# Optimization experiments

Hardware: AMD Instinct MI355X
Metric: run time of the kernel (lower is better)

Reference implementation:

```python
import jax, jax.numpy as jnp
import numpy as np


def setup_inputs() -> dict:
    key = jax.random.key(0)
    k1, k2 = jax.random.split(key)
    x = jax.random.normal(k1, (32, 512, 384), dtype=jnp.float32)
    duration = jax.random.randint(k2, (32, 512), 0, 16, dtype=jnp.int32)
    return {"x": x, "duration": duration, "max_len": 4096}


def reference(x, duration, max_len):
    # x: [B, T, D] phoneme encodings; duration: [B, T] nonneg frame counts.
    # Equivalent to repeat_interleave(x, duration, axis=1) then pad/truncate to max_len.
    dur = jnp.maximum(duration, 0)
    cs = jnp.cumsum(dur, axis=1)                      # [B, T] cumulative end offsets
    t = jnp.arange(max_len, dtype=cs.dtype)          # [L] output frame positions
    # frame t belongs to phoneme i iff cs[i-1] <= t < cs[i]
    idx = jax.vmap(lambda c: jnp.searchsorted(c, t, side="right"))(cs)  # [B, L]
    total = cs[:, -1]                                 # [B] expanded lengths (mel_len)
    valid = t[None, :] < total[:, None]               # [B, L] frames beyond total are padding
    idx = jnp.minimum(idx, x.shape[1] - 1)
    out = jnp.take_along_axis(x, idx[:, :, None], axis=1)   # [B, L, D] gather
    out = jnp.where(valid[:, :, None], out, jnp.zeros((), dtype=x.dtype))
    return out, total
```

## Files before the change

### kernel.cpp

```cpp
#include <hip/hip_runtime.h>
#include <hip/hip_bf16.h>


#define B      32
#define S      512
#define T      4096
#define D      384
#define D4     96
#define TILE_T 64

__global__ __launch_bounds__(256) void lr_fused_kernel(
    const float4* __restrict__ x,
    const int*    __restrict__ duration,
    float4*       __restrict__ out,
    float*        __restrict__ total_out)
{
    const int blk = blockIdx.x;
    const int b   = blk >> 6;
    const int t0  = (blk & 63) * TILE_T;
    const int tid = threadIdx.x;

    __shared__ int s_cs[S];
    __shared__ int s_p[256];
    __shared__ int s_idx[TILE_T];

    const int2 d2 = ((const int2*)(duration + b * S))[tid];
    const int a0 = max(d2.x, 0);
    const int a1 = max(d2.y, 0);
    s_p[tid] = a0 + a1;
    __syncthreads();

    #pragma unroll
    for (int off = 1; off < 256; off <<= 1) {
        int v = (tid >= off) ? s_p[tid - off] : 0;
        __syncthreads();
        s_p[tid] += v;
        __syncthreads();
    }

    const int P = s_p[tid];
    s_cs[2 * tid]     = P - a1;
    s_cs[2 * tid + 1] = P;
    __syncthreads();

    const int total = s_cs[S - 1];

    if (t0 == 0 && tid == 0) {
        total_out[b] = (float)total;
    }

    if (tid < TILE_T) {
        const int t = t0 + tid;
        int idx = -1;
        if (t < total) {
            int lo = 0;
            #pragma unroll
            for (int step = 256; step > 0; step >>= 1) {
                int mid = lo + step;
                if (mid <= S && s_cs[mid - 1] <= t) lo = mid;
            }
            idx = min(lo, S - 1);
        }
        s_idx[tid] = idx;
    }
    __syncthreads();

    const float4* xb = x   + (size_t)b * S * D4;
    float4*       ob = out + ((size_t)b * T + t0) * D4;

    #pragma unroll 4
    for (int e = tid; e < TILE_T * D4; e += 256) {
        const int r = e / D4;
        const int c = e - r * D4;
        const int idx = s_idx[r];
        float4 v;
        if (idx < 0) {
            v = make_float4(0.f, 0.f, 0.f, 0.f);
        } else {
            v = xb[idx * D4 + c];
        }
        ob[r * D4 + c] = v;
    }
}

extern "C" void kernel_launch(void* const* d_in, const int* in_sizes, int n_in,
                              void* d_out, int out_size, void* d_ws, size_t ws_size,
                              hipStream_t stream) {
    const float* x        = (const float*)d_in[0];
    const int*   duration = (const int*)d_in[1];

    float* out      = (float*)d_out;
    float* total_of = out + (size_t)B * T * D;

    const int nblocks = B * (T / TILE_T);
    lr_fused_kernel<<<nblocks, 256, 0, stream>>>(
        (const float4*)x, duration, (float4*)out, total_of);
}
```

Before: 40.69 us.

## Use wave-shuffle scan, XCD-aware block remap, larger tiles and nontemporal stores

Replaces the shared-memory Hillis-Steele prefix scan, which needs many barriers, with a wavefront shuffle scan plus a small cross-wave combine. Doubles the time tile to 128 frames so each block does more output work per scan. Remaps block IDs so consecutive logical tiles of a batch land on the same XCD, aiming to improve L2 reuse of the x rows. Writes output with nontemporal stores to avoid polluting cache with the large streaming output. The cost is fewer blocks and possibly lower occupancy and parallelism.

```diff
diff --git a/kernel.cpp b/kernel.cpp
--- a/kernel.cpp
+++ b/kernel.cpp
@@ -7,45 +7,56 @@
 #define T      4096
 #define D      384
 #define D4     96
-#define TILE_T 64
+#define TILE_T 128
+#define TILES_PER_B (T / TILE_T)
+#define NBLK   (B * TILES_PER_B)
+#define NXCD   8
+
+typedef float vfloat4 __attribute__((ext_vector_type(4)));
 
 __global__ __launch_bounds__(256) void lr_fused_kernel(
-    const float4* __restrict__ x,
+    const vfloat4* __restrict__ x,
     const int*    __restrict__ duration,
-    float4*       __restrict__ out,
+    vfloat4*      __restrict__ out,
     float*        __restrict__ total_out)
 {
-    const int blk = blockIdx.x;
-    const int b   = blk >> 6;
-    const int t0  = (blk & 63) * TILE_T;
-    const int tid = threadIdx.x;
+    const int raw     = blockIdx.x;
+    const int logical = (raw & (NXCD - 1)) * (NBLK / NXCD) + (raw >> 3);
+
+    const int b    = logical >> 5;
+    const int tile = logical & 31;
+    const int t0   = tile * TILE_T;
+    const int tid  = threadIdx.x;
+    const int lane = tid & 63;
+    const int wid  = tid >> 6;
 
     __shared__ int s_cs[S];
-    __shared__ int s_p[256];
+    __shared__ int s_wsum[4];
     __shared__ int s_idx[TILE_T];
 
     const int2 d2 = ((const int2*)(duration + b * S))[tid];
-    const int a0 = max(d2.x, 0);
     const int a1 = max(d2.y, 0);
-    s_p[tid] = a0 + a1;
+    int p = max(d2.x, 0) + a1;
+
+    #pragma unroll
+    for (int off = 1; off < 64; off <<= 1) {
+        int v = __shfl_up(p, off, 64);
+        if (lane >= off) p += v;
+    }
+    if (lane == 63) s_wsum[wid] = p;
     __syncthreads();
 
+    int prefix = 0;
     #pragma unroll
-    for (int off = 1; off < 256; off <<= 1) {
-        int v = (tid >= off) ? s_p[tid - off] : 0;
-        __syncthreads();
-        s_p[tid] += v;
-        __syncthreads();
-    }
+    for (int w = 0; w < 3; ++w) prefix += (w < wid) ? s_wsum[w] : 0;
 
-    const int P = s_p[tid];
+    const int P = p + prefix;
     s_cs[2 * tid]     = P - a1;
     s_cs[2 * tid + 1] = P;
     __syncthreads();
 
     const int total = s_cs[S - 1];
-
-    if (t0 == 0 && tid == 0) {
+    if (tile == 0 && tid == 0) {
         total_out[b] = (float)total;
     }
 
@@ -65,21 +76,21 @@
     }
     __syncthreads();
 
-    const float4* xb = x   + (size_t)b * S * D4;
-    float4*       ob = out + ((size_t)b * T + t0) * D4;
+    const vfloat4* xb = x   + (size_t)b * S * D4;
+    vfloat4*       ob = out + ((size_t)b * T + t0) * D4;
 
     #pragma unroll 4
     for (int e = tid; e < TILE_T * D4; e += 256) {
         const int r = e / D4;
         const int c = e - r * D4;
         const int idx = s_idx[r];
-        float4 v;
+        vfloat4 v;
         if (idx < 0) {
-            v = make_float4(0.f, 0.f, 0.f, 0.f);
+            v = (vfloat4)(0.f);
         } else {
             v = xb[idx * D4 + c];
         }
-        ob[r * D4 + c] = v;
+        __builtin_nontemporal_store(v, &ob[r * D4 + c]);
     }
 }
 
@@ -92,7 +103,6 @@
     float* out      = (float*)d_out;
     float* total_of = out + (size_t)B * T * D;
 
-    const int nblocks = B * (T / TILE_T);
-    lr_fused_kernel<<<nblocks, 256, 0, stream>>>(
-        (const float4*)x, duration, (float4*)out, total_of);
+    lr_fused_kernel<<<NBLK, 256, 0, stream>>>(
+        (const vfloat4*)x, duration, (vfloat4*)out, total_of);
 }
```

After: 45.63 us. +12.1%, slower.
